# Kernel optimization log

Hardware: AMD Instinct MI355X
Metric: run time of the kernel (lower is better)

## Reference

```python
import jax, jax.numpy as jnp
import numpy as np

B, F, D = 2048, 40, 32
CIN = (64, 64)


def _glorot(key, shape):
    fan_in, fan_out = shape[1] * shape[2], shape[0] * shape[2]
    std = jnp.sqrt(2.0 / (fan_in + fan_out)).astype(jnp.float32)
    return jax.random.normal(key, shape, dtype=jnp.float32) * std


def setup_inputs() -> dict:
    key = jax.random.key(0)
    kx, k0, k1 = jax.random.split(key, 3)
    x = jax.random.normal(kx, (B, F, D), dtype=jnp.float32)
    W0 = _glorot(k0, (CIN[0], F * F, D))
    b0 = jnp.zeros((CIN[0],), dtype=jnp.float32)
    W1 = _glorot(k1, (CIN[1], F * CIN[0], D))
    b1 = jnp.zeros((CIN[1],), dtype=jnp.float32)
    return {"x": x, "W0": W0, "b0": b0, "W1": W1, "b1": b1}


def _cin_step(x0, xk, W, b):
    # x0: (B,F,D)  xk: (B,H,D)  W: (O, H*F, D)  b: (O,)
    Bn, H, Dn = xk.shape
    Fn = x0.shape[1]
    # outer product per embedding channel, h-major flatten as in tf.reshape
    z = jnp.einsum('bhd,bfd->bhfd', xk, x0).reshape(Bn, H * Fn, Dn)
    # per-embedding-channel contraction against weights: (B,D,O)
    y = jnp.einsum('bhd,ohd->bdo', z, W) + b
    y = jax.nn.relu(y)
    return jnp.transpose(y, (0, 2, 1))  # (B,O,D)


def reference(x, W0, b0, W1, b1):
    x1 = _cin_step(x, x, W0, b0)
    x2 = _cin_step(x, x1, W1, b1)
    final = jnp.concatenate([x, x1, x2], axis=1)  # (B, F+O0+O1, D)
    return jnp.sum(final, axis=-1)  # (B, F+O0+O1)
```

## Files before the change

kernel.cpp:

```cpp
#include <hip/hip_runtime.h>

typedef unsigned int   u32;
typedef unsigned short u16;
typedef _Float16       f16;

using f16x8  = __attribute__((ext_vector_type(8)))  _Float16;
using f32x16 = __attribute__((ext_vector_type(16))) float;

#define LLDS16(G, L) __builtin_amdgcn_global_load_lds( \
  (const __attribute__((address_space(1))) u32*)(G), \
  (__attribute__((address_space(3))) u32*)(L), 16, 0, 0)

#define WAITV(N) { asm volatile("s_waitcnt vmcnt(" #N ")" ::: "memory"); \
                   __builtin_amdgcn_sched_barrier(0); }
#define FENCE_BAR() { asm volatile("s_waitcnt lgkmcnt(0)" ::: "memory"); \
                      __builtin_amdgcn_sched_barrier(0); \
                      __builtin_amdgcn_s_barrier(); \
                      __builtin_amdgcn_sched_barrier(0); }
#define BAR() { __builtin_amdgcn_s_barrier(); __builtin_amdgcn_sched_barrier(0); }
#define KEEP(x) asm volatile("" : "+v"(x))

__global__ __launch_bounds__(256)
void prep(const float* __restrict__ x,
          const float* __restrict__ W0, const float* __restrict__ W1,
          f16* __restrict__ xt, f16* __restrict__ W0p, f16* __restrict__ W1p,
          float* __restrict__ out){
  __shared__ char shm[33920];
  const int tid = threadIdx.x;
  if (blockIdx.x < 2560){
    float (*tile)[33] = (float(*)[33])shm;
    const int r0 = blockIdx.x << 5;
    const int c  = tid & 31;
    const int rp = tid >> 5;
#pragma unroll
    for (int p = 0; p < 4; ++p){
      const int r = (p << 3) + rp;
      float v = x[(size_t)(r0 + r) * 32 + c];
      tile[r][c] = v;
      float s = v;
#pragma unroll
      for (int off = 16; off > 0; off >>= 1) s += __shfl_xor(s, off, 32);
      if (c == 0){
        const int row = r0 + r;
        out[(size_t)(row / 40) * 168 + (row % 40)] = s;
      }
    }
    __syncthreads();
#pragma unroll
    for (int p = 0; p < 4; ++p){
      const int dd = (p << 3) + rp;
      xt[(size_t)dd * 81920 + r0 + c] = (f16)tile[c][dd];
    }
  } else {
    u16* t = (u16*)shm;
    int kb = blockIdx.x - 2560;
    const float* in; f16* outp; int K;
    if (kb < 200){ in = W0; outp = W0p; K = 1600; }
    else         { kb -= 200; in = W1; outp = W1p; K = 2560; }
    const int kbase = kb << 3;
#pragma unroll 4
    for (int i = 0; i < 64; ++i){
      const int idx = tid + (i << 8);
      const int o   = idx >> 8;
      const int rem = idx & 255;
      const int e   = rem >> 5;
      const int dd  = rem & 31;
      const float v = in[(size_t)o * (K * 32) + (size_t)(kbase + e) * 32 + dd];
      union { f16 h; u16 u; } cv; cv.h = (f16)v;
      t[dd * 530 + o * 8 + e] = cv.u;
    }
    __syncthreads();
    const u32* t32 = (const u32*)t;
    u32* o32 = (u32*)outp;
    const int obase = kb << 8;
#pragma unroll 4
    for (int i = 0; i < 32; ++i){
      const int idx = tid + (i << 8);
      const int dd  = idx >> 8;
      const int rem = idx & 255;
      o32[(size_t)dd * (K * 32) + obase + rem] = t32[dd * 265 + rem];
    }
  }
}

__global__ __launch_bounds__(512, 1)
void cin_fused(const f16* __restrict__ xt,
               const f16* __restrict__ W0p,
               const f16* __restrict__ W1p,
               const float* __restrict__ b0v, const float* __restrict__ b1v,
               f16* __restrict__ x1s,
               f16* __restrict__ y2s){
  constexpr int X0OFF = 81920;
  constexpr int X1OFF = 110592;
  constexpr int X0MS  = 32 * 112;
  constexpr int X1MS  = 32 * 144;

  const int bid = blockIdx.x;
  const int d   = ((bid & 7) << 2) | ((bid >> 3) & 3);
  const int b0  = (bid >> 5) << 8;
  const int tid = threadIdx.x;
  const int wv  = tid >> 6;
  const int wr  = wv >> 1;
  const int wc  = wv & 1;
  const int l   = tid & 63;
  const int hi  = l >> 5;
  const int lr  = l & 31;

  __shared__ char smem[147456];

  const f16* gW0 = W0p + (size_t)d * 102400;
  const f16* gW1 = W1p + (size_t)d * 163840;

#define ISSUE(I) do { \
    const f16* src_ = ((I) < 5) ? (gW0 + (size_t)(I) * 20480) \
                                : (gW1 + (size_t)((I) - 5) * 20480); \
    const f16* gt_ = src_ + wv * 2560 + l * 8; \
    char* lb_ = smem + ((I) & 1) * 40960 + wv * 5120; \
    _Pragma("unroll") \
    for (int j_ = 0; j_ < 5; ++j_) LLDS16(gt_ + j_ * 512, lb_ + j_ * 1024); \
  } while (0)

  ISSUE(0);
  ISSUE(1);

  {
    const uint4* src = (const uint4*)(xt + (size_t)d * 81920 + (size_t)b0 * 40);
#pragma unroll
    for (int it = 0; it < 3; ++it){
      const int idx = tid + (it << 9);
      if (idx < 1280){
        const int r = idx / 5, c = idx - r * 5;
        *(uint4*)(smem + X0OFF + r * 112 + c * 16) = src[idx];
      }
    }
  }
  __syncthreads();

  const char* x0row = smem + X0OFF + (wr * 64 + lr) * 112;
  const char* x1row = smem + X1OFF + (wr * 64 + lr) * 144;
  const int   hcol  = (wc << 5) + lr;
  const float bv1   = b0v[hcol];
  const float bv2   = b1v[hcol];

  f16x8 sl[2][5];
#pragma unroll
  for (int m = 0; m < 2; ++m){
    const char* xe = x0row + m * X0MS + hi * 16;
#pragma unroll
    for (int t = 0; t < 4; ++t) sl[m][t] = *(const f16x8*)(xe + t * 16);
    sl[m][4] = *(const f16x8*)(x0row + m * X0MS + (hi ? 0 : 64));
  }
  KEEP(sl[0][0]); KEEP(sl[0][1]); KEEP(sl[0][2]); KEEP(sl[0][3]); KEEP(sl[0][4]);
  KEEP(sl[1][0]); KEEP(sl[1][1]); KEEP(sl[1][2]); KEEP(sl[1][3]); KEEP(sl[1][4]);

  f32x16 acc0 = {0,0,0,0,0,0,0,0,0,0,0,0,0,0,0,0};
  f32x16 acc1 = {0,0,0,0,0,0,0,0,0,0,0,0,0,0,0,0};

  const int vb = hi * 1024 + wc * 512 + lr * 16;

  static constexpr int J0[10]  = {0,4,3,2,1,0,4,3,2,1};
  static constexpr int H0[10]  = {0,0,1,2,3,4,4,5,6,7};
  static constexpr int H0b[10] = {0,1,1,2,3,4,5,5,6,7};
  static constexpr int S0[10]  = {0,1,0,0,0,0,1,0,0,0};
  static constexpr int J2[10]  = {2,1,0,4,3,2,1,0,4,3};
  static constexpr int H2[10]  = {0,1,2,2,3,4,5,6,6,7};
  static constexpr int H2b[10] = {0,1,2,3,3,4,5,6,7,7};
  static constexpr int S2[10]  = {0,0,0,1,0,0,0,0,1,0};

#define COMP(BB) do { \
  _Pragma("unroll") \
  for (int si = 0; si < 10; ++si){ \
    const f16x8 bf0 = *(const f16x8*)((BB) + (si * 4) * 1024); \
    const f16x8 bf2 = *(const f16x8*)((BB) + (si * 4 + 2) * 1024); \
    const f16 xa00 = (S0[si] && hi) ? xh0[H0b[si]] : xh0[H0[si]]; \
    const f16 xa01 = (S0[si] && hi) ? xh1[H0b[si]] : xh1[H0[si]]; \
    const f16 xa20 = (S2[si] && hi) ? xh0[H2b[si]] : xh0[H2[si]]; \
    const f16 xa21 = (S2[si] && hi) ? xh1[H2b[si]] : xh1[H2[si]]; \
    acc0 = __builtin_amdgcn_mfma_f32_32x32x16_f16(sl[0][J0[si]] * xa00, bf0, acc0, 0, 0, 0); \
    acc1 = __builtin_amdgcn_mfma_f32_32x32x16_f16(sl[1][J0[si]] * xa01, bf0, acc1, 0, 0, 0); \
    acc0 = __builtin_amdgcn_mfma_f32_32x32x16_f16(sl[0][J2[si]] * xa20, bf2, acc0, 0, 0, 0); \
    acc1 = __builtin_amdgcn_mfma_f32_32x32x16_f16(sl[1][J2[si]] * xa21, bf2, acc1, 0, 0, 0); \
  } \
} while (0)

  {
    f16x8 xh0 = *(const f16x8*)(x0row);
    f16x8 xh1 = *(const f16x8*)(x0row + X0MS);
    for (int t = 0; t < 5; ++t){
      const char* bb = smem + (t & 1) * 40960 + vb;
      const f16x8 xhn0 = *(const f16x8*)(x0row + (t + 1) * 16);
      const f16x8 xhn1 = *(const f16x8*)(x0row + X0MS + (t + 1) * 16);
      COMP(bb);
      FENCE_BAR();
      ISSUE(t + 2);
      WAITV(5);
      BAR();
      xh0 = xhn0; xh1 = xhn1;
    }
  }

  {
    u16* x1w = (u16*)(smem + X1OFF);
#pragma unroll
    for (int m = 0; m < 2; ++m)
#pragma unroll
      for (int reg = 0; reg < 16; ++reg){
        const int row = (wr << 6) + (m << 5) + (reg & 3) + ((reg >> 2) << 3) + (hi << 2);
        float v = (m ? acc1[reg] : acc0[reg]) + bv1;
        v = v > 0.f ? v : 0.f;
        union { f16 h; u16 u; } cv; cv.h = (f16)v;
        x1w[row * 72 + hcol] = cv.u;
      }
    const f32x16 fz = {0,0,0,0,0,0,0,0,0,0,0,0,0,0,0,0};
    acc0 = fz; acc1 = fz;
    asm volatile("s_waitcnt lgkmcnt(0)" ::: "memory");
    __builtin_amdgcn_sched_barrier(0);
    WAITV(0);
    BAR();
#pragma unroll
    for (int it = 0; it < 4; ++it){
      const int u   = tid + (it << 9);
      const int row = u >> 3, ch = u & 7;
      const f16x8 vv = *(const f16x8*)((const char*)x1w + row * 144 + ch * 16);
      *(f16x8*)(x1s + (size_t)(b0 + row) * 2048 + d * 64 + ch * 8) = vv;
    }
  }

  {
    f16x8 xh0 = *(const f16x8*)(x1row);
    f16x8 xh1 = *(const f16x8*)(x1row + X1MS);
    for (int t = 0; t < 8; ++t){
      const char* bb = smem + ((t + 1) & 1) * 40960 + vb;
      const f16x8 xhn0 = *(const f16x8*)(x1row + (t + 1) * 16);
      const f16x8 xhn1 = *(const f16x8*)(x1row + X1MS + (t + 1) * 16);
      COMP(bb);
      FENCE_BAR();
      if (t + 2 < 8){
        ISSUE(5 + t + 2);
        WAITV(5);
      } else {
        WAITV(0);
      }
      BAR();
      xh0 = xhn0; xh1 = xhn1;
    }
  }

  {
    u16* yw = (u16*)(smem + X1OFF);
#pragma unroll
    for (int m = 0; m < 2; ++m)
#pragma unroll
      for (int reg = 0; reg < 16; ++reg){
        const int row = (wr << 6) + (m << 5) + (reg & 3) + ((reg >> 2) << 3) + (hi << 2);
        float v = (m ? acc1[reg] : acc0[reg]) + bv2;
        v = v > 0.f ? v : 0.f;
        union { f16 h; u16 u; } cv; cv.h = (f16)v;
        yw[row * 72 + hcol] = cv.u;
      }
    asm volatile("s_waitcnt lgkmcnt(0)" ::: "memory");
    __builtin_amdgcn_sched_barrier(0);
    BAR();
#pragma unroll
    for (int it = 0; it < 4; ++it){
      const int u   = tid + (it << 9);
      const int row = u >> 3, ch = u & 7;
      const f16x8 vv = *(const f16x8*)((const char*)yw + row * 144 + ch * 16);
      *(f16x8*)(y2s + (size_t)(b0 + row) * 2048 + d * 64 + ch * 8) = vv;
    }
  }
#undef ISSUE
#undef COMP
}

__global__ __launch_bounds__(128)
void finalize(const f16* __restrict__ x1s, const f16* __restrict__ y2s,
              float* __restrict__ out){
  const int b = blockIdx.x;
  const int t = threadIdx.x;
  if (t < 64){
    float s = 0.f;
#pragma unroll
    for (int d = 0; d < 32; ++d) s += (float)x1s[(size_t)b * 2048 + d * 64 + t];
    out[(size_t)b * 168 + 40 + t] = s;
  } else {
    const int o = t - 64;
    float s = 0.f;
#pragma unroll
    for (int d = 0; d < 32; ++d) s += (float)y2s[(size_t)b * 2048 + d * 64 + o];
    out[(size_t)b * 168 + 104 + o] = s;
  }
}

extern "C" void kernel_launch(void* const* d_in, const int* in_sizes, int n_in,
                              void* d_out, int out_size, void* d_ws, size_t ws_size,
                              hipStream_t stream){
  const float* x   = (const float*)d_in[0];
  const float* W0  = (const float*)d_in[1];
  const float* b0v = (const float*)d_in[2];
  const float* W1  = (const float*)d_in[3];
  const float* b1v = (const float*)d_in[4];
  float* out = (float*)d_out;

  char* ws = (char*)d_ws;
  f16* xt  = (f16*)(ws + 0);
  f16* W0p = (f16*)(ws + 5242880);
  f16* W1p = (f16*)(ws + 11796480);
  f16* x1s = (f16*)(ws + 22282240);
  f16* y2s = (f16*)(ws + 30670848);

  prep<<<3080, 256, 0, stream>>>(x, W0, W1, xt, W0p, W1p, out);
  cin_fused<<<256, 512, 0, stream>>>(xt, W0p, W1p, b0v, b1v, x1s, y2s);
  finalize<<<2048, 128, 0, stream>>>(x1s, y2s, out);
}
```

Before: 59.47 us.

## Switch fused CIN GEMM from 32x32x16 to 16x16x32 MFMA with wider row tiles

Reworks the fused CIN kernel to use 16x16x32 f16 MFMA instead of 32x32x16. Each wave now covers 128 batch rows by 16 output channels, with 8 accumulators, instead of 64 rows by 32 channels. The wave grid and x0 LDS row stride change to match, and the x-scalar broadcast tables are rebuilt for the new lane grouping. The aim is better reuse of each weight fragment across more MFMAs and a different LDS access pattern. In exchange it keeps many more preloaded x0 slices in registers (8x5 vectors), which raises register pressure, and it pins waves_per_eu to 2.

```diff
diff --git a/kernel.cpp b/kernel.cpp
--- a/kernel.cpp
+++ b/kernel.cpp
@@ -4,8 +4,8 @@
 typedef unsigned short u16;
 typedef _Float16       f16;
 
-using f16x8  = __attribute__((ext_vector_type(8)))  _Float16;
-using f32x16 = __attribute__((ext_vector_type(16))) float;
+using f16x8 = __attribute__((ext_vector_type(8))) _Float16;
+using f32x4 = __attribute__((ext_vector_type(4))) float;
 
 #define LLDS16(G, L) __builtin_amdgcn_global_load_lds( \
   (const __attribute__((address_space(1))) u32*)(G), \
@@ -83,6 +83,7 @@
   }
 }
 
+__attribute__((amdgpu_waves_per_eu(2, 2)))
 __global__ __launch_bounds__(512, 1)
 void cin_fused(const f16* __restrict__ xt,
                const f16* __restrict__ W0p,
@@ -91,22 +92,19 @@
                f16* __restrict__ x1s,
                f16* __restrict__ y2s){
   constexpr int X0OFF = 81920;
-  constexpr int X1OFF = 110592;
-  constexpr int X0MS  = 32 * 112;
-  constexpr int X1MS  = 32 * 144;
-
+  constexpr int X1OFF = 106496;
   const int bid = blockIdx.x;
   const int d   = ((bid & 7) << 2) | ((bid >> 3) & 3);
   const int b0  = (bid >> 5) << 8;
   const int tid = threadIdx.x;
   const int wv  = tid >> 6;
-  const int wr  = wv >> 1;
-  const int wc  = wv & 1;
+  const int rg  = wv >> 2;
+  const int cg  = wv & 3;
   const int l   = tid & 63;
-  const int hi  = l >> 5;
-  const int lr  = l & 31;
-
-  __shared__ char smem[147456];
+  const int lo  = l & 15;
+  const int g   = l >> 4;
+
+  __shared__ char smem[143360];
 
   const f16* gW0 = W0p + (size_t)d * 102400;
   const f16* gW1 = W1p + (size_t)d * 163840;
@@ -130,89 +128,84 @@
       const int idx = tid + (it << 9);
       if (idx < 1280){
         const int r = idx / 5, c = idx - r * 5;
-        *(uint4*)(smem + X0OFF + r * 112 + c * 16) = src[idx];
+        *(uint4*)(smem + X0OFF + r * 96 + c * 16) = src[idx];
       }
     }
   }
   __syncthreads();
 
-  const char* x0row = smem + X0OFF + (wr * 64 + lr) * 112;
-  const char* x1row = smem + X1OFF + (wr * 64 + lr) * 144;
-  const int   hcol  = (wc << 5) + lr;
-  const float bv1   = b0v[hcol];
-  const float bv2   = b1v[hcol];
-
-  f16x8 sl[2][5];
-#pragma unroll
-  for (int m = 0; m < 2; ++m){
-    const char* xe = x0row + m * X0MS + hi * 16;
-#pragma unroll
-    for (int t = 0; t < 4; ++t) sl[m][t] = *(const f16x8*)(xe + t * 16);
-    sl[m][4] = *(const f16x8*)(x0row + m * X0MS + (hi ? 0 : 64));
-  }
-  KEEP(sl[0][0]); KEEP(sl[0][1]); KEEP(sl[0][2]); KEEP(sl[0][3]); KEEP(sl[0][4]);
-  KEEP(sl[1][0]); KEEP(sl[1][1]); KEEP(sl[1][2]); KEEP(sl[1][3]); KEEP(sl[1][4]);
-
-  f32x16 acc0 = {0,0,0,0,0,0,0,0,0,0,0,0,0,0,0,0};
-  f32x16 acc1 = {0,0,0,0,0,0,0,0,0,0,0,0,0,0,0,0};
-
-  const int vb = hi * 1024 + wc * 512 + lr * 16;
-
-  static constexpr int J0[10]  = {0,4,3,2,1,0,4,3,2,1};
-  static constexpr int H0[10]  = {0,0,1,2,3,4,4,5,6,7};
-  static constexpr int H0b[10] = {0,1,1,2,3,4,5,5,6,7};
-  static constexpr int S0[10]  = {0,1,0,0,0,0,1,0,0,0};
-  static constexpr int J2[10]  = {2,1,0,4,3,2,1,0,4,3};
-  static constexpr int H2[10]  = {0,1,2,2,3,4,5,6,6,7};
-  static constexpr int H2b[10] = {0,1,2,3,3,4,5,6,7,7};
-  static constexpr int S2[10]  = {0,0,0,1,0,0,0,0,1,0};
-
-#define COMP(BB) do { \
+  const char* x0r = smem + X0OFF + ((rg << 7) + lo) * 96;
+  const char* x1r = smem + X1OFF + ((rg << 7) + lo) * 144;
+  const int   col = (cg << 4) + lo;
+  const float bv1 = b0v[col];
+  const float bv2 = b1v[col];
+
+  static constexpr int JT[5] = {0, 4, 3, 2, 1};
+  f16x8 sl[8][5];
+#pragma unroll
+  for (int m = 0; m < 8; ++m){
+    const char* rb = x0r + m * 1536;
+#pragma unroll
+    for (int t = 0; t < 5; ++t){
+      int j = JT[t] + g; if (j >= 5) j -= 5;
+      sl[m][t] = *(const f16x8*)(rb + j * 16);
+    }
+  }
+#pragma unroll
+  for (int m = 0; m < 8; ++m)
+#pragma unroll
+    for (int t = 0; t < 5; ++t) KEEP(sl[m][t]);
+
+  f32x4 acc[8];
+#pragma unroll
+  for (int m = 0; m < 8; ++m) acc[m] = (f32x4){0.f, 0.f, 0.f, 0.f};
+
+  const int vb = (g << 10) + (cg << 8) + (lo << 4);
+
+  static constexpr int SL[10] = {0,1,2,3,4,0,1,2,3,4};
+  static constexpr int EA[10] = {0,0,1,2,3,4,4,5,6,7};
+  static constexpr int EB[10] = {0,1,2,3,3,4,5,6,7,7};
+  static constexpr int TT[10] = {4,1,2,3,4,4,1,2,3,4};
+
+#define COMP(BB, XB, XMS, TI) do { \
+  f16x8 xh[8]; \
+  _Pragma("unroll") \
+  for (int m = 0; m < 8; ++m) \
+    xh[m] = *(const f16x8*)((XB) + m * (XMS) + (TI) * 16); \
   _Pragma("unroll") \
   for (int si = 0; si < 10; ++si){ \
-    const f16x8 bf0 = *(const f16x8*)((BB) + (si * 4) * 1024); \
-    const f16x8 bf2 = *(const f16x8*)((BB) + (si * 4 + 2) * 1024); \
-    const f16 xa00 = (S0[si] && hi) ? xh0[H0b[si]] : xh0[H0[si]]; \
-    const f16 xa01 = (S0[si] && hi) ? xh1[H0b[si]] : xh1[H0[si]]; \
-    const f16 xa20 = (S2[si] && hi) ? xh0[H2b[si]] : xh0[H2[si]]; \
-    const f16 xa21 = (S2[si] && hi) ? xh1[H2b[si]] : xh1[H2[si]]; \
-    acc0 = __builtin_amdgcn_mfma_f32_32x32x16_f16(sl[0][J0[si]] * xa00, bf0, acc0, 0, 0, 0); \
-    acc1 = __builtin_amdgcn_mfma_f32_32x32x16_f16(sl[1][J0[si]] * xa01, bf0, acc1, 0, 0, 0); \
-    acc0 = __builtin_amdgcn_mfma_f32_32x32x16_f16(sl[0][J2[si]] * xa20, bf2, acc0, 0, 0, 0); \
-    acc1 = __builtin_amdgcn_mfma_f32_32x32x16_f16(sl[1][J2[si]] * xa21, bf2, acc1, 0, 0, 0); \
+    const f16x8 bf = *(const f16x8*)((BB) + vb + si * 4096); \
+    _Pragma("unroll") \
+    for (int m = 0; m < 8; ++m){ \
+      const f16 xa = (g >= TT[si]) ? xh[m][EB[si]] : xh[m][EA[si]]; \
+      const f16x8 av = sl[m][SL[si]] * xa; \
+      acc[m] = __builtin_amdgcn_mfma_f32_16x16x32_f16(av, bf, acc[m], 0, 0, 0); \
+    } \
   } \
 } while (0)
 
-  {
-    f16x8 xh0 = *(const f16x8*)(x0row);
-    f16x8 xh1 = *(const f16x8*)(x0row + X0MS);
-    for (int t = 0; t < 5; ++t){
-      const char* bb = smem + (t & 1) * 40960 + vb;
-      const f16x8 xhn0 = *(const f16x8*)(x0row + (t + 1) * 16);
-      const f16x8 xhn1 = *(const f16x8*)(x0row + X0MS + (t + 1) * 16);
-      COMP(bb);
-      FENCE_BAR();
-      ISSUE(t + 2);
-      WAITV(5);
-      BAR();
-      xh0 = xhn0; xh1 = xhn1;
-    }
+  for (int t = 0; t < 5; ++t){
+    const char* bb = smem + (t & 1) * 40960;
+    COMP(bb, x0r, 1536, t);
+    FENCE_BAR();
+    ISSUE(t + 2);
+    WAITV(5);
+    BAR();
   }
 
   {
     u16* x1w = (u16*)(smem + X1OFF);
 #pragma unroll
-    for (int m = 0; m < 2; ++m)
-#pragma unroll
-      for (int reg = 0; reg < 16; ++reg){
-        const int row = (wr << 6) + (m << 5) + (reg & 3) + ((reg >> 2) << 3) + (hi << 2);
-        float v = (m ? acc1[reg] : acc0[reg]) + bv1;
+    for (int m = 0; m < 8; ++m)
+#pragma unroll
+      for (int r = 0; r < 4; ++r){
+        const int row = (rg << 7) + (m << 4) + (g << 2) + r;
+        float v = acc[m][r] + bv1;
         v = v > 0.f ? v : 0.f;
         union { f16 h; u16 u; } cv; cv.h = (f16)v;
-        x1w[row * 72 + hcol] = cv.u;
+        x1w[row * 72 + col] = cv.u;
+        acc[m][r] = 0.f;
       }
-    const f32x16 fz = {0,0,0,0,0,0,0,0,0,0,0,0,0,0,0,0};
-    acc0 = fz; acc1 = fz;
     asm volatile("s_waitcnt lgkmcnt(0)" ::: "memory");
     __builtin_amdgcn_sched_barrier(0);
     WAITV(0);
@@ -226,37 +219,30 @@
     }
   }
 
-  {
-    f16x8 xh0 = *(const f16x8*)(x1row);
-    f16x8 xh1 = *(const f16x8*)(x1row + X1MS);
-    for (int t = 0; t < 8; ++t){
-      const char* bb = smem + ((t + 1) & 1) * 40960 + vb;
-      const f16x8 xhn0 = *(const f16x8*)(x1row + (t + 1) * 16);
-      const f16x8 xhn1 = *(const f16x8*)(x1row + X1MS + (t + 1) * 16);
-      COMP(bb);
-      FENCE_BAR();
-      if (t + 2 < 8){
-        ISSUE(5 + t + 2);
-        WAITV(5);
-      } else {
-        WAITV(0);
-      }
-      BAR();
-      xh0 = xhn0; xh1 = xhn1;
-    }
+  for (int t = 0; t < 8; ++t){
+    const char* bb = smem + ((t + 1) & 1) * 40960;
+    COMP(bb, x1r, 2304, t);
+    FENCE_BAR();
+    if (t + 2 < 8){
+      ISSUE(7 + t);
+      WAITV(5);
+    } else {
+      WAITV(0);
+    }
+    BAR();
   }
 
   {
     u16* yw = (u16*)(smem + X1OFF);
 #pragma unroll
-    for (int m = 0; m < 2; ++m)
-#pragma unroll
-      for (int reg = 0; reg < 16; ++reg){
-        const int row = (wr << 6) + (m << 5) + (reg & 3) + ((reg >> 2) << 3) + (hi << 2);
-        float v = (m ? acc1[reg] : acc0[reg]) + bv2;
+    for (int m = 0; m < 8; ++m)
+#pragma unroll
+      for (int r = 0; r < 4; ++r){
+        const int row = (rg << 7) + (m << 4) + (g << 2) + r;
+        float v = acc[m][r] + bv2;
         v = v > 0.f ? v : 0.f;
         union { f16 h; u16 u; } cv; cv.h = (f16)v;
-        yw[row * 72 + hcol] = cv.u;
+        yw[row * 72 + col] = cv.u;
       }
     asm volatile("s_waitcnt lgkmcnt(0)" ::: "memory");
     __builtin_amdgcn_sched_barrier(0);
```

After: 196.2 us. 3.3x slower.

## Halve CIN block tile so two blocks co-reside per CU, add MFMA priority

Applied to the files above, without the earlier changes.

The fused CIN kernel now processes 128 batch rows per block with 256 threads instead of 256 rows with 512 threads, and launches 512 blocks with launch bounds allowing two per CU. Weight pipeline stages shrink to half size, which doubles the stage count, and LDS per block roughly halves so two blocks fit. The aim is to let independent blocks overlap one block's barriers and weight loads with the other's MFMA work; s_setprio around the compute loop favours MFMA issue. The cost is twice as many barriers and stage handoffs, and each weight slice is loaded by twice as many blocks.

```diff
diff --git a/kernel.cpp b/kernel.cpp
--- a/kernel.cpp
+++ b/kernel.cpp
@@ -5,6 +5,7 @@
 typedef _Float16       f16;
 
 using f16x8  = __attribute__((ext_vector_type(8)))  _Float16;
+using f16x4  = __attribute__((ext_vector_type(4)))  _Float16;
 using f32x16 = __attribute__((ext_vector_type(16))) float;
 
 #define LLDS16(G, L) __builtin_amdgcn_global_load_lds( \
@@ -83,21 +84,21 @@
   }
 }
 
-__global__ __launch_bounds__(512, 1)
+__global__ __launch_bounds__(256, 2)
 void cin_fused(const f16* __restrict__ xt,
                const f16* __restrict__ W0p,
                const f16* __restrict__ W1p,
                const float* __restrict__ b0v, const float* __restrict__ b1v,
                f16* __restrict__ x1s,
                f16* __restrict__ y2s){
-  constexpr int X0OFF = 81920;
-  constexpr int X1OFF = 110592;
-  constexpr int X0MS  = 32 * 112;
+  constexpr int X0OFF = 40960;
+  constexpr int X1OFF = 53248;
+  constexpr int X0MS  = 32 * 96;
   constexpr int X1MS  = 32 * 144;
 
   const int bid = blockIdx.x;
   const int d   = ((bid & 7) << 2) | ((bid >> 3) & 3);
-  const int b0  = (bid >> 5) << 8;
+  const int b0  = (bid >> 5) << 7;
   const int tid = threadIdx.x;
   const int wv  = tid >> 6;
   const int wr  = wv >> 1;
@@ -106,16 +107,16 @@
   const int hi  = l >> 5;
   const int lr  = l & 31;
 
-  __shared__ char smem[147456];
+  __shared__ char smem[71680];
 
   const f16* gW0 = W0p + (size_t)d * 102400;
   const f16* gW1 = W1p + (size_t)d * 163840;
 
 #define ISSUE(I) do { \
-    const f16* src_ = ((I) < 5) ? (gW0 + (size_t)(I) * 20480) \
-                                : (gW1 + (size_t)((I) - 5) * 20480); \
+    const f16* src_ = ((I) < 10) ? (gW0 + (size_t)(I) * 10240) \
+                                 : (gW1 + (size_t)((I) - 10) * 10240); \
     const f16* gt_ = src_ + wv * 2560 + l * 8; \
-    char* lb_ = smem + ((I) & 1) * 40960 + wv * 5120; \
+    char* lb_ = smem + ((I) & 1) * 20480 + wv * 5120; \
     _Pragma("unroll") \
     for (int j_ = 0; j_ < 5; ++j_) LLDS16(gt_ + j_ * 512, lb_ + j_ * 1024); \
   } while (0)
@@ -127,28 +128,28 @@
     const uint4* src = (const uint4*)(xt + (size_t)d * 81920 + (size_t)b0 * 40);
 #pragma unroll
     for (int it = 0; it < 3; ++it){
-      const int idx = tid + (it << 9);
-      if (idx < 1280){
+      const int idx = tid + (it << 8);
+      if (idx < 640){
         const int r = idx / 5, c = idx - r * 5;
-        *(uint4*)(smem + X0OFF + r * 112 + c * 16) = src[idx];
+        *(uint4*)(smem + X0OFF + r * 96 + c * 16) = src[idx];
       }
     }
   }
   __syncthreads();
 
-  const char* x0row = smem + X0OFF + (wr * 64 + lr) * 112;
-  const char* x1row = smem + X1OFF + (wr * 64 + lr) * 144;
-  const int   hcol  = (wc << 5) + lr;
-  const float bv1   = b0v[hcol];
-  const float bv2   = b1v[hcol];
+  const char* x0r = smem + X0OFF + ((wr << 6) + lr) * 96;
+  const char* x1r = smem + X1OFF + ((wr << 6) + lr) * 144;
+  const int   col = (wc << 5) + lr;
+  const float bv1 = b0v[col];
+  const float bv2 = b1v[col];
 
   f16x8 sl[2][5];
 #pragma unroll
   for (int m = 0; m < 2; ++m){
-    const char* xe = x0row + m * X0MS + hi * 16;
+    const char* xe = x0r + m * X0MS + hi * 16;
 #pragma unroll
     for (int t = 0; t < 4; ++t) sl[m][t] = *(const f16x8*)(xe + t * 16);
-    sl[m][4] = *(const f16x8*)(x0row + m * X0MS + (hi ? 0 : 64));
+    sl[m][4] = *(const f16x8*)(x0r + m * X0MS + (hi ? 0 : 64));
   }
   KEEP(sl[0][0]); KEEP(sl[0][1]); KEEP(sl[0][2]); KEEP(sl[0][3]); KEEP(sl[0][4]);
   KEEP(sl[1][0]); KEEP(sl[1][1]); KEEP(sl[1][2]); KEEP(sl[1][3]); KEEP(sl[1][4]);
@@ -156,22 +157,23 @@
   f32x16 acc0 = {0,0,0,0,0,0,0,0,0,0,0,0,0,0,0,0};
   f32x16 acc1 = {0,0,0,0,0,0,0,0,0,0,0,0,0,0,0,0};
 
-  const int vb = hi * 1024 + wc * 512 + lr * 16;
-
-  static constexpr int J0[10]  = {0,4,3,2,1,0,4,3,2,1};
-  static constexpr int H0[10]  = {0,0,1,2,3,4,4,5,6,7};
-  static constexpr int H0b[10] = {0,1,1,2,3,4,5,5,6,7};
-  static constexpr int S0[10]  = {0,1,0,0,0,0,1,0,0,0};
-  static constexpr int J2[10]  = {2,1,0,4,3,2,1,0,4,3};
-  static constexpr int H2[10]  = {0,1,2,2,3,4,5,6,6,7};
-  static constexpr int H2b[10] = {0,1,2,3,3,4,5,6,7,7};
-  static constexpr int S2[10]  = {0,0,0,1,0,0,0,0,1,0};
+  const int vb = (hi << 10) + (wc << 9) + (lr << 4);
+
+  static constexpr int J0[5]  = {0, 4, 3, 2, 1};
+  static constexpr int H0[5]  = {0, 0, 1, 2, 3};
+  static constexpr int H0b[5] = {0, 1, 1, 2, 3};
+  static constexpr int S0[5]  = {0, 1, 0, 0, 0};
+  static constexpr int J2[5]  = {2, 1, 0, 4, 3};
+  static constexpr int H2[5]  = {0, 1, 2, 2, 3};
+  static constexpr int H2b[5] = {0, 1, 2, 3, 3};
+  static constexpr int S2[5]  = {0, 0, 0, 1, 0};
 
 #define COMP(BB) do { \
+  __builtin_amdgcn_s_setprio(1); \
   _Pragma("unroll") \
-  for (int si = 0; si < 10; ++si){ \
-    const f16x8 bf0 = *(const f16x8*)((BB) + (si * 4) * 1024); \
-    const f16x8 bf2 = *(const f16x8*)((BB) + (si * 4 + 2) * 1024); \
+  for (int si = 0; si < 5; ++si){ \
+    const f16x8 bf0 = *(const f16x8*)((BB) + vb + (si * 4) * 1024); \
+    const f16x8 bf2 = *(const f16x8*)((BB) + vb + (si * 4 + 2) * 1024); \
     const f16 xa00 = (S0[si] && hi) ? xh0[H0b[si]] : xh0[H0[si]]; \
     const f16 xa01 = (S0[si] && hi) ? xh1[H0b[si]] : xh1[H0[si]]; \
     const f16 xa20 = (S2[si] && hi) ? xh0[H2b[si]] : xh0[H2[si]]; \
@@ -181,15 +183,16 @@
     acc0 = __builtin_amdgcn_mfma_f32_32x32x16_f16(sl[0][J2[si]] * xa20, bf2, acc0, 0, 0, 0); \
     acc1 = __builtin_amdgcn_mfma_f32_32x32x16_f16(sl[1][J2[si]] * xa21, bf2, acc1, 0, 0, 0); \
   } \
+  __builtin_amdgcn_s_setprio(0); \
 } while (0)
 
   {
-    f16x8 xh0 = *(const f16x8*)(x0row);
-    f16x8 xh1 = *(const f16x8*)(x0row + X0MS);
-    for (int t = 0; t < 5; ++t){
-      const char* bb = smem + (t & 1) * 40960 + vb;
-      const f16x8 xhn0 = *(const f16x8*)(x0row + (t + 1) * 16);
-      const f16x8 xhn1 = *(const f16x8*)(x0row + X0MS + (t + 1) * 16);
+    f16x4 xh0 = *(const f16x4*)(x0r);
+    f16x4 xh1 = *(const f16x4*)(x0r + X0MS);
+    for (int t = 0; t < 10; ++t){
+      const char* bb = smem + (t & 1) * 20480;
+      const f16x4 xhn0 = *(const f16x4*)(x0r + (t + 1) * 8);
+      const f16x4 xhn1 = *(const f16x4*)(x0r + X0MS + (t + 1) * 8);
       COMP(bb);
       FENCE_BAR();
       ISSUE(t + 2);
@@ -209,7 +212,7 @@
         float v = (m ? acc1[reg] : acc0[reg]) + bv1;
         v = v > 0.f ? v : 0.f;
         union { f16 h; u16 u; } cv; cv.h = (f16)v;
-        x1w[row * 72 + hcol] = cv.u;
+        x1w[row * 72 + col] = cv.u;
       }
     const f32x16 fz = {0,0,0,0,0,0,0,0,0,0,0,0,0,0,0,0};
     acc0 = fz; acc1 = fz;
@@ -219,7 +222,7 @@
     BAR();
 #pragma unroll
     for (int it = 0; it < 4; ++it){
-      const int u   = tid + (it << 9);
+      const int u   = tid + (it << 8);
       const int row = u >> 3, ch = u & 7;
       const f16x8 vv = *(const f16x8*)((const char*)x1w + row * 144 + ch * 16);
       *(f16x8*)(x1s + (size_t)(b0 + row) * 2048 + d * 64 + ch * 8) = vv;
@@ -227,16 +230,16 @@
   }
 
   {
-    f16x8 xh0 = *(const f16x8*)(x1row);
-    f16x8 xh1 = *(const f16x8*)(x1row + X1MS);
-    for (int t = 0; t < 8; ++t){
-      const char* bb = smem + ((t + 1) & 1) * 40960 + vb;
-      const f16x8 xhn0 = *(const f16x8*)(x1row + (t + 1) * 16);
-      const f16x8 xhn1 = *(const f16x8*)(x1row + X1MS + (t + 1) * 16);
+    f16x4 xh0 = *(const f16x4*)(x1r);
+    f16x4 xh1 = *(const f16x4*)(x1r + X1MS);
+    for (int t = 0; t < 16; ++t){
+      const char* bb = smem + (t & 1) * 20480;
+      const f16x4 xhn0 = *(const f16x4*)(x1r + (t + 1) * 8);
+      const f16x4 xhn1 = *(const f16x4*)(x1r + X1MS + (t + 1) * 8);
       COMP(bb);
       FENCE_BAR();
-      if (t + 2 < 8){
-        ISSUE(5 + t + 2);
+      if (t + 2 < 16){
+        ISSUE(12 + t);
         WAITV(5);
       } else {
         WAITV(0);
@@ -256,14 +259,14 @@
         float v = (m ? acc1[reg] : acc0[reg]) + bv2;
         v = v > 0.f ? v : 0.f;
         union { f16 h; u16 u; } cv; cv.h = (f16)v;
-        yw[row * 72 + hcol] = cv.u;
+        yw[row * 72 + col] = cv.u;
       }
     asm volatile("s_waitcnt lgkmcnt(0)" ::: "memory");
     __builtin_amdgcn_sched_barrier(0);
     BAR();
 #pragma unroll
     for (int it = 0; it < 4; ++it){
-      const int u   = tid + (it << 9);
+      const int u   = tid + (it << 8);
       const int row = u >> 3, ch = u & 7;
       const f16x8 vv = *(const f16x8*)((const char*)yw + row * 144 + ch * 16);
       *(f16x8*)(y2s + (size_t)(b0 + row) * 2048 + d * 64 + ch * 8) = vv;
@@ -310,6 +313,6 @@
   f16* y2s = (f16*)(ws + 30670848);
 
   prep<<<3080, 256, 0, stream>>>(x, W0, W1, xt, W0p, W1p, out);
-  cin_fused<<<256, 512, 0, stream>>>(xt, W0p, W1p, b0v, b1v, x1s, y2s);
+  cin_fused<<<512, 256, 0, stream>>>(xt, W0p, W1p, b0v, b1v, x1s, y2s);
   finalize<<<2048, 128, 0, stream>>>(x1s, y2s, out);
 }
```

Measured after the change: 59.80 us. About the same (+0.5%).
